# Optimization experiments

Hardware: AMD Instinct MI355X
Metric: run time of the kernel (lower is better)

The kernel has to match this reference:

```python
import jax, jax.numpy as jnp
import numpy as np

EMBED_DIM = 1024
NUM_TOKENS = 32
TOKEN_DIM = 32  # ceil(1024/32)
CODEBOOK_SIZE = 256
BATCH = 32768
BETA = 0.25


def setup_inputs() -> dict:
    key = jax.random.key(0)
    ks = jax.random.split(key, 6)
    lim_e = 1.0 / np.sqrt(EMBED_DIM)
    lim_d = 1.0 / np.sqrt(NUM_TOKENS * TOKEN_DIM)
    lim_c = 1.0 / CODEBOOK_SIZE
    return {
        "skills": jax.random.normal(ks[0], (BATCH, EMBED_DIM), jnp.float32),
        "enc_w": jax.random.uniform(ks[1], (NUM_TOKENS * TOKEN_DIM, EMBED_DIM), jnp.float32, -lim_e, lim_e),
        "enc_b": jax.random.uniform(ks[2], (NUM_TOKENS * TOKEN_DIM,), jnp.float32, -lim_e, lim_e),
        "codebook": jax.random.uniform(ks[3], (CODEBOOK_SIZE, TOKEN_DIM), jnp.float32, -lim_c, lim_c),
        "dec_w": jax.random.uniform(ks[4], (EMBED_DIM, NUM_TOKENS * TOKEN_DIM), jnp.float32, -lim_d, lim_d),
        "dec_b": jax.random.uniform(ks[5], (EMBED_DIM,), jnp.float32, -lim_d, lim_d),
    }


def reference(skills, enc_w, enc_b, codebook, dec_w, dec_b):
    B = skills.shape[0]
    # encoder linear -> [B, num_tokens, token_dim]
    projected = (skills @ enc_w.T + enc_b).reshape(B, NUM_TOKENS, TOKEN_DIM)
    flat = projected.reshape(-1, TOKEN_DIM)  # [B*T, d]
    # squared-euclidean distances to codebook entries: [B*T, K]
    dists = (
        jnp.sum(flat * flat, axis=1, keepdims=True)
        - 2.0 * flat @ codebook.T
        + jnp.sum(codebook * codebook, axis=1)[None, :]
    )
    codes = jnp.argmin(dists, axis=1)  # [B*T]
    quantized = codebook[codes].reshape(B, NUM_TOKENS, TOKEN_DIM)
    # straight-through estimator
    st = projected + jax.lax.stop_gradient(quantized - projected)
    commitment = jnp.mean((projected - jax.lax.stop_gradient(quantized)) ** 2)
    codebook_loss = jnp.mean((quantized - jax.lax.stop_gradient(projected)) ** 2)
    vq_loss = codebook_loss + BETA * commitment
    reconstructed = st.reshape(B, NUM_TOKENS * TOKEN_DIM) @ dec_w.T + dec_b
    recon_loss = jnp.mean((reconstructed - skills) ** 2)
    loss = vq_loss + recon_loss
    return reconstructed, codes.reshape(B, NUM_TOKENS), loss
```

## Files before the change

kernel.cpp:

```cpp
#include <hip/hip_runtime.h>
#include <hip/hip_bf16.h>
#include <float.h>

#define NROWS 32768
#define EMB 1024
#define CBN 256
#define TD 32

#define OUT_CODES_OFF (33554432UL)
#define OUT_LOSS_OFF  (34603008UL)
#define TAU 1e-5f
#define INV_N (1.0f/33554432.0f)

typedef __attribute__((ext_vector_type(8))) short s16x8;
typedef __attribute__((ext_vector_type(4))) float f32x4;

__device__ __forceinline__ unsigned short bf16r(float x) {
    unsigned int u = __float_as_uint(x);
    unsigned int r = (u + 0x7FFFu + ((u >> 16) & 1u)) >> 16;
    return (unsigned short)r;
}
__device__ __forceinline__ float bf16f(unsigned short h) {
    return __uint_as_float(((unsigned int)h) << 16);
}
__device__ __forceinline__ void split8r(float4 v0, float4 v1, s16x8& h, s16x8& l) {
    float xs[8] = {v0.x, v0.y, v0.z, v0.w, v1.x, v1.y, v1.z, v1.w};
    #pragma unroll
    for (int e = 0; e < 8; ++e) {
        unsigned int u = __float_as_uint(xs[e]);
        unsigned short hh = (unsigned short)(u >> 16);
        h[e] = (short)hh;
        l[e] = (short)bf16r(xs[e] - bf16f(hh));
    }
}

__global__ void k_prep(const float* __restrict__ in,
                       unsigned short* __restrict__ hi,
                       unsigned short* __restrict__ lo,
                       int n8)
{
    const int i = blockIdx.x * 256 + threadIdx.x;
    if (i >= n8) return;
    const float4* p = (const float4*)(in + (size_t)i * 8);
    s16x8 h, l;
    split8r(p[0], p[1], h, l);
    *(s16x8*)(hi + (size_t)i * 8) = h;
    *(s16x8*)(lo + (size_t)i * 8) = l;
}

template <bool PREW>
__launch_bounds__(512, 1)
__global__ void k_enc(const unsigned short* __restrict__ s_hi,
                      const unsigned short* __restrict__ s_lo,
                      const float* __restrict__ enc_w,
                      const unsigned short* __restrict__ w_hi,
                      const unsigned short* __restrict__ w_lo,
                      const float* __restrict__ enc_b,
                      const float* __restrict__ cb_g,
                      float* __restrict__ out)
{
    __shared__ __align__(16) char smem[125952];
    typedef unsigned short (*pu40)[40];
    pu40 Ah = (pu40)(smem);
    pu40 Al = (pu40)(smem + 10240);
    pu40 Bh = (pu40)(smem + 20480);
    pu40 Bl = (pu40)(smem + 30720);
    pu40 Sh = (pu40)(smem);
    pu40 Sl = (pu40)(smem + 40960);
    pu40 Ch = (pu40)(smem + 81920);
    pu40 Cl = (pu40)(smem + 102400);
    float* cnb = (float*)(smem + 122880);
    float* Fv  = (float*)(smem + 123904);

    const int tid = threadIdx.x;
    const int r0 = blockIdx.x * 128;
    const int wid = tid >> 6, lane = tid & 63;
    const int wm = wid >> 1, wn = wid & 1;
    const int mbase = wm * 32, nbase = wn * 64;
    const int lhi = lane >> 4, llo = lane & 15;
    const int srow = tid >> 2, sq = tid & 3;

    if (tid < 256) {
        const float4* cr = (const float4*)&cb_g[tid * 32];
        float s = 0.f;
        #pragma unroll
        for (int i = 0; i < 8; ++i) {
            float4 v = cr[i];
            float c[4] = {v.x, v.y, v.z, v.w};
            #pragma unroll
            for (int e = 0; e < 4; ++e) {
                unsigned int u = __float_as_uint(c[e]);
                unsigned short hh = (unsigned short)(u >> 16);
                Ch[tid][i*4+e] = hh;
                Cl[tid][i*4+e] = bf16r(c[e] - bf16f(hh));
                s = fmaf(c[e], c[e], s);
            }
        }
        cnb[tid] = s;
    }
    __syncthreads();

    float vq_local = 0.f;
    f32x4 acc[2][4];
    s16x8 rah, ral, rbh, rbl;

    {
        const size_t aoff = (size_t)(r0 + srow) * 1024 + sq * 8;
        rah = *(const s16x8*)(s_hi + aoff);
        ral = *(const s16x8*)(s_lo + aoff);
        if (PREW) {
            const size_t boff = (size_t)srow * 1024 + sq * 8;
            rbh = *(const s16x8*)(w_hi + boff);
            rbl = *(const s16x8*)(w_lo + boff);
        } else {
            const float* bp = &enc_w[(size_t)srow * 1024 + sq * 8];
            split8r(*(const float4*)bp, *(const float4*)(bp + 4), rbh, rbl);
        }
    }

    for (int it = 0; it < 256; ++it) {
        const int nt = it >> 5, kt = it & 31;
        const int n0 = nt * 128;
        if (kt == 0) {
            #pragma unroll
            for (int mf = 0; mf < 2; ++mf)
                #pragma unroll
                for (int nf = 0; nf < 4; ++nf) acc[mf][nf] = (f32x4)0.f;
        }
        __syncthreads();
        *(s16x8*)&Ah[srow][sq * 8] = rah;
        *(s16x8*)&Al[srow][sq * 8] = ral;
        *(s16x8*)&Bh[srow][sq * 8] = rbh;
        *(s16x8*)&Bl[srow][sq * 8] = rbl;
        __syncthreads();
        if (it < 255) {
            const int it2 = it + 1, nt2 = it2 >> 5, kt2 = it2 & 31;
            const size_t aoff = (size_t)(r0 + srow) * 1024 + kt2 * 32 + sq * 8;
            rah = *(const s16x8*)(s_hi + aoff);
            ral = *(const s16x8*)(s_lo + aoff);
            if (PREW) {
                const size_t boff = (size_t)(nt2 * 128 + srow) * 1024 + kt2 * 32 + sq * 8;
                rbh = *(const s16x8*)(w_hi + boff);
                rbl = *(const s16x8*)(w_lo + boff);
            } else {
                const float* bp = &enc_w[(size_t)(nt2 * 128 + srow) * 1024 + kt2 * 32 + sq * 8];
                split8r(*(const float4*)bp, *(const float4*)(bp + 4), rbh, rbl);
            }
        }
        {
            s16x8 ah[2], al[2], bh[4], bl[4];
            #pragma unroll
            for (int mf = 0; mf < 2; ++mf) {
                const int row = mbase + mf * 16 + llo;
                ah[mf] = *(s16x8*)&Ah[row][lhi * 8];
                al[mf] = *(s16x8*)&Al[row][lhi * 8];
            }
            #pragma unroll
            for (int nf = 0; nf < 4; ++nf) {
                const int row = nbase + nf * 16 + llo;
                bh[nf] = *(s16x8*)&Bh[row][lhi * 8];
                bl[nf] = *(s16x8*)&Bl[row][lhi * 8];
            }
            #pragma unroll
            for (int mf = 0; mf < 2; ++mf)
                #pragma unroll
                for (int nf = 0; nf < 4; ++nf) {
                    acc[mf][nf] = __builtin_amdgcn_mfma_f32_16x16x32_bf16(ah[mf], bh[nf], acc[mf][nf], 0, 0, 0);
                    acc[mf][nf] = __builtin_amdgcn_mfma_f32_16x16x32_bf16(ah[mf], bl[nf], acc[mf][nf], 0, 0, 0);
                    acc[mf][nf] = __builtin_amdgcn_mfma_f32_16x16x32_bf16(al[mf], bh[nf], acc[mf][nf], 0, 0, 0);
                }
        }

        if (kt == 31) {
            __syncthreads();
            float fp[2][4][2];
            #pragma unroll
            for (int mf = 0; mf < 2; ++mf)
                #pragma unroll
                for (int r = 0; r < 4; ++r) { fp[mf][r][0] = 0.f; fp[mf][r][1] = 0.f; }

            #pragma unroll
            for (int mf = 0; mf < 2; ++mf)
                #pragma unroll
                for (int nf = 0; nf < 4; ++nf) {
                    const int n_local = nbase + nf * 16 + llo;
                    const float bias = enc_b[n0 + n_local];
                    const int tl = wn * 2 + (nf >> 1);
                    const int d = ((nf & 1) << 4) + llo;
                    #pragma unroll
                    for (int r = 0; r < 4; ++r) {
                        const int m_local = mbase + mf * 16 + lhi * 4 + r;
                        float val = acc[mf][nf][r] + bias;
                        unsigned int u = __float_as_uint(val);
                        unsigned short hh = (unsigned short)(u >> 16);
                        Sh[m_local * 4 + tl][d] = hh;
                        Sl[m_local * 4 + tl][d] = bf16r(val - bf16f(hh));
                        fp[mf][r][nf >> 1] = fmaf(val, val, fp[mf][r][nf >> 1]);
                    }
                }
            #pragma unroll
            for (int mf = 0; mf < 2; ++mf)
                #pragma unroll
                for (int r = 0; r < 4; ++r)
                    #pragma unroll
                    for (int tt = 0; tt < 2; ++tt) {
                        float f = fp[mf][r][tt];
                        f += __shfl_xor(f, 1); f += __shfl_xor(f, 2);
                        f += __shfl_xor(f, 4); f += __shfl_xor(f, 8);
                        if (llo == 0)
                            Fv[(mbase + mf * 16 + lhi * 4 + r) * 4 + wn * 2 + tt] = f;
                    }
            __syncthreads();

            #pragma unroll
            for (int gi = 0; gi < 4; ++gi) {
                const int g = wid * 4 + gi;
                const int tokrow = g * 16 + llo;
                s16x8 fh = *(s16x8*)&Sh[tokrow][lhi * 8];
                s16x8 fl = *(s16x8*)&Sl[tokrow][lhi * 8];
                float s1[4], s2[4]; int bj[4];
                #pragma unroll
                for (int r = 0; r < 4; ++r) { s1[r] = FLT_MAX; s2[r] = FLT_MAX; bj[r] = 0; }
                for (int jb = 0; jb < 16; ++jb) {
                    const int j = jb * 16 + llo;
                    s16x8 ch = *(s16x8*)&Ch[j][lhi * 8];
                    s16x8 cl = *(s16x8*)&Cl[j][lhi * 8];
                    f32x4 sc = (f32x4)0.f;
                    sc = __builtin_amdgcn_mfma_f32_16x16x32_bf16(fh, ch, sc, 0, 0, 0);
                    sc = __builtin_amdgcn_mfma_f32_16x16x32_bf16(fh, cl, sc, 0, 0, 0);
                    sc = __builtin_amdgcn_mfma_f32_16x16x32_bf16(fl, ch, sc, 0, 0, 0);
                    const float cnv = cnb[j];
                    #pragma unroll
                    for (int r = 0; r < 4; ++r) {
                        float s = fmaf(-2.f, sc[r], cnv);
                        if (s < s1[r])      { s2[r] = s1[r]; s1[r] = s; bj[r] = j; }
                        else if (s < s2[r]) { s2[r] = s; }
                    }
                }
                #pragma unroll
                for (int r = 0; r < 4; ++r) {
                    float a1 = s1[r], a2 = s2[r]; int aj = bj[r];
                    #pragma unroll
                    for (int off = 1; off <= 8; off <<= 1) {
                        float o1 = __shfl_xor(a1, off);
                        float o2 = __shfl_xor(a2, off);
                        int   oj = __shfl_xor(aj, off);
                        if (o1 < a1) { a2 = fminf(a1, o2); a1 = o1; aj = oj; }
                        else         { a2 = fminf(o1, a2); }
                    }
                    if (llo == 0) {
                        const int tok_local = g * 16 + lhi * 4 + r;
                        const float F = Fv[tok_local];
                        float cv = (a2 - a1 < TAU) ? (float)(aj + 512) : (float)aj;
                        const size_t tok = (size_t)(r0 + (tok_local >> 2)) * 32 + nt * 4 + (tok_local & 3);
                        out[OUT_CODES_OFF + tok] = cv;
                        vq_local += F + a1;
                    }
                }
            }
        }
    }
    {
        float v = vq_local;
        #pragma unroll
        for (int off = 32; off >= 1; off >>= 1) v += __shfl_xor(v, off);
        if (lane == 0) atomicAdd(&out[OUT_LOSS_OFF], v * (1.25f * INV_N));
    }
}

__launch_bounds__(256)
__global__ void k_fix(const float* __restrict__ skills,
                      const float* __restrict__ enc_w,
                      const float* __restrict__ enc_b,
                      const float* __restrict__ cb_g,
                      float* __restrict__ codes)
{
    __shared__ unsigned int cnt;
    __shared__ unsigned short list[256];

    const int tid = threadIdx.x;
    const int base = blockIdx.x * 256;

    if (tid == 0) cnt = 0;
    __syncthreads();
    {
        const int c = (int)codes[base + tid];
        if (c >= 512) {
            unsigned int ix = atomicAdd(&cnt, 1u);
            list[ix] = (unsigned short)tid;
        }
    }
    __syncthreads();
    const unsigned int n = cnt;
    if (n == 0) return;

    const int wv = tid >> 6, lane = tid & 63;
    const int d = lane & 31;

    for (unsigned int i = wv; i < n; i += 4) {
        const int tok = base + (int)list[i];
        const int row = tok >> 5;
        const int t   = tok & 31;

        const float4* s4 = (const float4*)&skills[(size_t)row * 1024];
        const float4* w4 = (const float4*)&enc_w[(size_t)(t * 32 + d) * 1024];
        float v1 = 0.f, v2 = 0.f, v3 = 0.f;
        for (int q = 0; q < 96; ++q) {
            float4 a = s4[q], b = w4[q];
            v1 = fmaf(a.x, b.x, v1); v1 = fmaf(a.y, b.y, v1);
            v1 = fmaf(a.z, b.z, v1); v1 = fmaf(a.w, b.w, v1);
        }
        for (int q = 96; q < 192; ++q) {
            float4 a = s4[q], b = w4[q];
            v2 = fmaf(a.x, b.x, v2); v2 = fmaf(a.y, b.y, v2);
            v2 = fmaf(a.z, b.z, v2); v2 = fmaf(a.w, b.w, v2);
        }
        for (int q = 192; q < 256; ++q) {
            float4 a = s4[q], b = w4[q];
            v3 = fmaf(a.x, b.x, v3); v3 = fmaf(a.y, b.y, v3);
            v3 = fmaf(a.z, b.z, v3); v3 = fmaf(a.w, b.w, v3);
        }
        const float pd = ((v1 + v2) + v3) + enc_b[t * 32 + d];

        float pv[32];
        #pragma unroll
        for (int dd = 0; dd < 32; ++dd) pv[dd] = __shfl(pd, dd);

        float F;
        {
            float s[32];
            #pragma unroll
            for (int dd = 0; dd < 32; ++dd) s[dd] = pv[dd] * pv[dd];
            float r[8];
            #pragma unroll
            for (int j = 0; j < 8; ++j) r[j] = ((s[j] + s[8+j]) + s[16+j]) + s[24+j];
            F = ((r[0] + r[1]) + (r[2] + r[3])) + ((r[4] + r[5]) + (r[6] + r[7]));
        }

        float bs = FLT_MAX; int bj = 0;
        for (int m = 0; m < 4; ++m) {
            const int j = m * 64 + lane;
            const float* cj = &cb_g[j * 32];
            float g = 0.f;
            #pragma unroll
            for (int dd = 0; dd < 32; ++dd) g = fmaf(pv[dd], cj[dd], g);
            float cs[32];
            #pragma unroll
            for (int dd = 0; dd < 32; ++dd) cs[dd] = cj[dd] * cj[dd];
            float r[8];
            #pragma unroll
            for (int jj = 0; jj < 8; ++jj) r[jj] = ((cs[jj] + cs[8+jj]) + cs[16+jj]) + cs[24+jj];
            float cn = ((r[0] + r[1]) + (r[2] + r[3])) + ((r[4] + r[5]) + (r[6] + r[7]));
            float dist = (F - 2.0f * g) + cn;
            if (dist < bs) { bs = dist; bj = j; }
        }
        #pragma unroll
        for (int off = 32; off >= 1; off >>= 1) {
            float os = __shfl_xor(bs, off);
            int   oj = __shfl_xor(bj, off);
            if (os < bs || (os == bs && oj < bj)) { bs = os; bj = oj; }
        }
        if (lane == 0) codes[tok] = (float)bj;
    }
}

__launch_bounds__(512)
__global__ void k_dec(const float* __restrict__ skills,
                      const float* __restrict__ cb_g,
                      const float* __restrict__ dec_w,
                      const float* __restrict__ dec_b,
                      const float* __restrict__ codes,
                      float* __restrict__ recon,
                      float* __restrict__ loss_out)
{
    __shared__ unsigned short Qt[128][40], Wt[128][40];

    const int tid = threadIdx.x;
    const int r0 = (blockIdx.x >> 3) * 128;
    const int n0 = (blockIdx.x & 7) * 128;
    const int wid = tid >> 6, lane = tid & 63;
    const int wm = wid >> 1, wn = wid & 1;
    const int mbase = wm * 32, nbase = wn * 64;
    const int lhi = lane >> 4, llo = lane & 15;
    const int srow = tid >> 2, sq = tid & 3;

    f32x4 acc[2][4];
    #pragma unroll
    for (int mf = 0; mf < 2; ++mf)
        #pragma unroll
        for (int nf = 0; nf < 4; ++nf) acc[mf][nf] = (f32x4)0.f;

    float4 q0, q1, w0, w1;
    int cnext;
    {
        const int c0 = ((int)codes[(size_t)(r0 + srow) * 32 + 0]) & 255;
        const float* cp = &cb_g[c0 * 32 + sq * 8];
        q0 = *(const float4*)cp; q1 = *(const float4*)(cp + 4);
        const float* wp = &dec_w[(size_t)(n0 + srow) * 1024 + sq * 8];
        w0 = *(const float4*)wp; w1 = *(const float4*)(wp + 4);
        cnext = ((int)codes[(size_t)(r0 + srow) * 32 + 1]) & 255;
    }

    for (int t = 0; t < 32; ++t) {
        __syncthreads();
        {
            float xs[8] = {q0.x, q0.y, q0.z, q0.w, q1.x, q1.y, q1.z, q1.w};
            s16x8 h;
            #pragma unroll
            for (int e = 0; e < 8; ++e) h[e] = (short)bf16r(xs[e]);
            *(s16x8*)&Qt[srow][sq * 8] = h;
            float ys[8] = {w0.x, w0.y, w0.z, w0.w, w1.x, w1.y, w1.z, w1.w};
            #pragma unroll
            for (int e = 0; e < 8; ++e) h[e] = (short)bf16r(ys[e]);
            *(s16x8*)&Wt[srow][sq * 8] = h;
        }
        __syncthreads();
        if (t < 31) {
            const float* cp = &cb_g[cnext * 32 + sq * 8];
            q0 = *(const float4*)cp; q1 = *(const float4*)(cp + 4);
            const float* wp = &dec_w[(size_t)(n0 + srow) * 1024 + (t + 1) * 32 + sq * 8];
            w0 = *(const float4*)wp; w1 = *(const float4*)(wp + 4);
            if (t < 30) cnext = ((int)codes[(size_t)(r0 + srow) * 32 + t + 2]) & 255;
        }
        s16x8 aq[2], bw[4];
        #pragma unroll
        for (int mf = 0; mf < 2; ++mf)
            aq[mf] = *(s16x8*)&Qt[mbase + mf * 16 + llo][lhi * 8];
        #pragma unroll
        for (int nf = 0; nf < 4; ++nf)
            bw[nf] = *(s16x8*)&Wt[nbase + nf * 16 + llo][lhi * 8];
        #pragma unroll
        for (int mf = 0; mf < 2; ++mf)
            #pragma unroll
            for (int nf = 0; nf < 4; ++nf)
                acc[mf][nf] = __builtin_amdgcn_mfma_f32_16x16x32_bf16(aq[mf], bw[nf], acc[mf][nf], 0, 0, 0);
    }

    float lsum = 0.f;
    #pragma unroll
    for (int mf = 0; mf < 2; ++mf)
        #pragma unroll
        for (int nf = 0; nf < 4; ++nf) {
            const int col = n0 + nbase + nf * 16 + llo;
            const float bias = dec_b[col];
            #pragma unroll
            for (int r = 0; r < 4; ++r) {
                const int row = r0 + mbase + mf * 16 + lhi * 4 + r;
                float rv = acc[mf][nf][r] + bias;
                float dv = rv - skills[(size_t)row * 1024 + col];
                lsum = fmaf(dv, dv, lsum);
                recon[(size_t)row * 1024 + col] = rv;
            }
        }
    #pragma unroll
    for (int off = 32; off >= 1; off >>= 1) lsum += __shfl_xor(lsum, off);
    if (lane == 0) atomicAdd(loss_out, lsum * INV_N);
}

extern "C" void kernel_launch(void* const* d_in, const int* in_sizes, int n_in,
                              void* d_out, int out_size, void* d_ws, size_t ws_size,
                              hipStream_t stream)
{
    const float* skills = (const float*)d_in[0];
    const float* enc_w  = (const float*)d_in[1];
    const float* enc_b  = (const float*)d_in[2];
    const float* cbg    = (const float*)d_in[3];
    const float* dec_w  = (const float*)d_in[4];
    const float* dec_b  = (const float*)d_in[5];
    float* out = (float*)d_out;

    unsigned short* s_hi = (unsigned short*)out;
    unsigned short* s_lo = s_hi + 33554432UL;

    hipMemsetAsync(out + OUT_LOSS_OFF, 0, 4, stream);
    k_prep<<<dim3(16384), dim3(256), 0, stream>>>(skills, s_hi, s_lo, 4194304);

    const bool prew = (ws_size >= (4UL * 1048576UL + 64UL));
    unsigned short* w_hi = (unsigned short*)d_ws;
    unsigned short* w_lo = w_hi + 1048576UL;
    if (prew) {
        k_prep<<<dim3(512), dim3(256), 0, stream>>>(enc_w, w_hi, w_lo, 131072);
        k_enc<true><<<dim3(256), dim3(512), 0, stream>>>(s_hi, s_lo, enc_w, w_hi, w_lo,
                                                         enc_b, cbg, out);
    } else {
        k_enc<false><<<dim3(256), dim3(512), 0, stream>>>(s_hi, s_lo, enc_w, w_hi, w_lo,
                                                          enc_b, cbg, out);
    }
    k_fix<<<dim3(4096), dim3(256), 0, stream>>>(skills, enc_w, enc_b, cbg, out + OUT_CODES_OFF);
    k_dec<<<dim3(2048), dim3(512), 0, stream>>>(skills, cbg, dec_w, dec_b,
                                                out + OUT_CODES_OFF, out, out + OUT_LOSS_OFF);
}
```

Baseline: 947.1 us.

## Fuse skills bf16 split into encoder, widen N tile to 256, swizzle LDS

Removes the separate k_prep pass over skills, which wrote hi/lo bf16 copies. The encoder now loads fp32 skills directly and splits them in registers before the LDS store. The encoder N tile doubles to 256 (8 MFMA fragments per wave), halving the number of passes over the A rows. LDS uses an XOR-swizzled layout without padding, shrinking shared memory so launch bounds can allow 2 blocks per CU. The codebook argmin runs in two halves per 256-wide tile, which adds syncs and register pressure.

```diff
diff --git a/kernel.cpp b/kernel.cpp
--- a/kernel.cpp
+++ b/kernel.cpp
@@ -1,11 +1,6 @@
 #include <hip/hip_runtime.h>
 #include <hip/hip_bf16.h>
 #include <float.h>
-
-#define NROWS 32768
-#define EMB 1024
-#define CBN 256
-#define TD 32
 
 #define OUT_CODES_OFF (33554432UL)
 #define OUT_LOSS_OFF  (34603008UL)
@@ -49,9 +44,8 @@
 }
 
 template <bool PREW>
-__launch_bounds__(512, 1)
-__global__ void k_enc(const unsigned short* __restrict__ s_hi,
-                      const unsigned short* __restrict__ s_lo,
+__launch_bounds__(512, 2)
+__global__ void k_enc(const float* __restrict__ skills,
                       const float* __restrict__ enc_w,
                       const unsigned short* __restrict__ w_hi,
                       const unsigned short* __restrict__ w_lo,
@@ -59,26 +53,18 @@
                       const float* __restrict__ cb_g,
                       float* __restrict__ out)
 {
-    __shared__ __align__(16) char smem[125952];
-    typedef unsigned short (*pu40)[40];
-    pu40 Ah = (pu40)(smem);
-    pu40 Al = (pu40)(smem + 10240);
-    pu40 Bh = (pu40)(smem + 20480);
-    pu40 Bl = (pu40)(smem + 30720);
-    pu40 Sh = (pu40)(smem);
-    pu40 Sl = (pu40)(smem + 40960);
-    pu40 Ch = (pu40)(smem + 81920);
-    pu40 Cl = (pu40)(smem + 102400);
-    float* cnb = (float*)(smem + 122880);
-    float* Fv  = (float*)(smem + 123904);
+    __shared__ __align__(16) unsigned short us[50688];
+    float* cnb = (float*)(us + 49152);
+    float* Fv  = (float*)(us + 49664);
 
     const int tid = threadIdx.x;
     const int r0 = blockIdx.x * 128;
     const int wid = tid >> 6, lane = tid & 63;
     const int wm = wid >> 1, wn = wid & 1;
-    const int mbase = wm * 32, nbase = wn * 64;
+    const int mbase = wm * 32;
     const int lhi = lane >> 4, llo = lane & 15;
-    const int srow = tid >> 2, sq = tid & 3;
+    const int rowA = tid >> 2, kcA = tid & 3;
+    const int rowB = tid & 255, selB = tid >> 8;
 
     if (tid < 256) {
         const float4* cr = (const float4*)&cb_g[tid * 32];
@@ -89,10 +75,12 @@
             float c[4] = {v.x, v.y, v.z, v.w};
             #pragma unroll
             for (int e = 0; e < 4; ++e) {
+                const int d = i * 4 + e, kc = d >> 3, e8 = d & 7;
+                const int phys = tid ^ (kc << 2);
                 unsigned int u = __float_as_uint(c[e]);
                 unsigned short hh = (unsigned short)(u >> 16);
-                Ch[tid][i*4+e] = hh;
-                Cl[tid][i*4+e] = bf16r(c[e] - bf16f(hh));
+                us[8 * (4096 + kc * 256 + phys) + e8] = hh;
+                us[8 * (5120 + kc * 256 + phys) + e8] = bf16r(c[e] - bf16f(hh));
                 s = fmaf(c[e], c[e], s);
             }
         }
@@ -101,162 +89,196 @@
     __syncthreads();
 
     float vq_local = 0.f;
-    f32x4 acc[2][4];
-    s16x8 rah, ral, rbh, rbl;
+    f32x4 acc[2][8];
+    float4 pa0, pa1;
+    s16x8 pb[4];
+    float4 pbf[4];
 
     {
-        const size_t aoff = (size_t)(r0 + srow) * 1024 + sq * 8;
-        rah = *(const s16x8*)(s_hi + aoff);
-        ral = *(const s16x8*)(s_lo + aoff);
+        const float* ap = &skills[(size_t)(r0 + rowA) * 1024 + kcA * 8];
+        pa0 = *(const float4*)ap; pa1 = *(const float4*)(ap + 4);
         if (PREW) {
-            const size_t boff = (size_t)srow * 1024 + sq * 8;
-            rbh = *(const s16x8*)(w_hi + boff);
-            rbl = *(const s16x8*)(w_lo + boff);
+            const unsigned short* wp = (selB ? w_lo : w_hi) + (size_t)rowB * 1024;
+            #pragma unroll
+            for (int kc = 0; kc < 4; ++kc) pb[kc] = *(const s16x8*)(wp + kc * 8);
         } else {
-            const float* bp = &enc_w[(size_t)srow * 1024 + sq * 8];
-            split8r(*(const float4*)bp, *(const float4*)(bp + 4), rbh, rbl);
-        }
-    }
-
-    for (int it = 0; it < 256; ++it) {
+            const float* bp = &enc_w[(size_t)rowB * 1024 + selB * 16];
+            #pragma unroll
+            for (int q = 0; q < 4; ++q) pbf[q] = ((const float4*)bp)[q];
+        }
+    }
+
+    for (int it = 0; it < 128; ++it) {
         const int nt = it >> 5, kt = it & 31;
-        const int n0 = nt * 128;
+        const int n0 = nt * 256;
         if (kt == 0) {
             #pragma unroll
             for (int mf = 0; mf < 2; ++mf)
                 #pragma unroll
-                for (int nf = 0; nf < 4; ++nf) acc[mf][nf] = (f32x4)0.f;
+                for (int nf = 0; nf < 8; ++nf) acc[mf][nf] = (f32x4)0.f;
         }
         __syncthreads();
-        *(s16x8*)&Ah[srow][sq * 8] = rah;
-        *(s16x8*)&Al[srow][sq * 8] = ral;
-        *(s16x8*)&Bh[srow][sq * 8] = rbh;
-        *(s16x8*)&Bl[srow][sq * 8] = rbl;
+        {
+            s16x8 h, l; split8r(pa0, pa1, h, l);
+            const int phys = rowA ^ (kcA << 2);
+            *(s16x8*)(us + 8 * (kcA * 128 + phys)) = h;
+            *(s16x8*)(us + 8 * (512 + kcA * 128 + phys)) = l;
+        }
+        if (PREW) {
+            const int base = selB ? 2048 : 1024;
+            #pragma unroll
+            for (int kc = 0; kc < 4; ++kc) {
+                const int phys = rowB ^ (kc << 2);
+                *(s16x8*)(us + 8 * (base + kc * 256 + phys)) = pb[kc];
+            }
+        } else {
+            #pragma unroll
+            for (int kk = 0; kk < 2; ++kk) {
+                const int kc = selB * 2 + kk;
+                s16x8 h, l; split8r(pbf[kk * 2], pbf[kk * 2 + 1], h, l);
+                const int phys = rowB ^ (kc << 2);
+                *(s16x8*)(us + 8 * (1024 + kc * 256 + phys)) = h;
+                *(s16x8*)(us + 8 * (2048 + kc * 256 + phys)) = l;
+            }
+        }
         __syncthreads();
-        if (it < 255) {
+        if (it < 127) {
             const int it2 = it + 1, nt2 = it2 >> 5, kt2 = it2 & 31;
-            const size_t aoff = (size_t)(r0 + srow) * 1024 + kt2 * 32 + sq * 8;
-            rah = *(const s16x8*)(s_hi + aoff);
-            ral = *(const s16x8*)(s_lo + aoff);
+            const float* ap = &skills[(size_t)(r0 + rowA) * 1024 + kt2 * 32 + kcA * 8];
+            pa0 = *(const float4*)ap; pa1 = *(const float4*)(ap + 4);
             if (PREW) {
-                const size_t boff = (size_t)(nt2 * 128 + srow) * 1024 + kt2 * 32 + sq * 8;
-                rbh = *(const s16x8*)(w_hi + boff);
-                rbl = *(const s16x8*)(w_lo + boff);
+                const unsigned short* wp = (selB ? w_lo : w_hi)
+                    + (size_t)(nt2 * 256 + rowB) * 1024 + kt2 * 32;
+                #pragma unroll
+                for (int kc = 0; kc < 4; ++kc) pb[kc] = *(const s16x8*)(wp + kc * 8);
             } else {
-                const float* bp = &enc_w[(size_t)(nt2 * 128 + srow) * 1024 + kt2 * 32 + sq * 8];
-                split8r(*(const float4*)bp, *(const float4*)(bp + 4), rbh, rbl);
+                const float* bp = &enc_w[(size_t)(nt2 * 256 + rowB) * 1024 + kt2 * 32 + selB * 16];
+                #pragma unroll
+                for (int q = 0; q < 4; ++q) pbf[q] = ((const float4*)bp)[q];
             }
         }
         {
-            s16x8 ah[2], al[2], bh[4], bl[4];
+            s16x8 ah[2], al[2];
             #pragma unroll
             for (int mf = 0; mf < 2; ++mf) {
-                const int row = mbase + mf * 16 + llo;
-                ah[mf] = *(s16x8*)&Ah[row][lhi * 8];
-                al[mf] = *(s16x8*)&Al[row][lhi * 8];
-            }
-            #pragma unroll
-            for (int nf = 0; nf < 4; ++nf) {
-                const int row = nbase + nf * 16 + llo;
-                bh[nf] = *(s16x8*)&Bh[row][lhi * 8];
-                bl[nf] = *(s16x8*)&Bl[row][lhi * 8];
-            }
-            #pragma unroll
-            for (int mf = 0; mf < 2; ++mf)
-                #pragma unroll
-                for (int nf = 0; nf < 4; ++nf) {
-                    acc[mf][nf] = __builtin_amdgcn_mfma_f32_16x16x32_bf16(ah[mf], bh[nf], acc[mf][nf], 0, 0, 0);
-                    acc[mf][nf] = __builtin_amdgcn_mfma_f32_16x16x32_bf16(ah[mf], bl[nf], acc[mf][nf], 0, 0, 0);
-                    acc[mf][nf] = __builtin_amdgcn_mfma_f32_16x16x32_bf16(al[mf], bh[nf], acc[mf][nf], 0, 0, 0);
+                const int phys = (mbase + mf * 16 + llo) ^ (lhi << 2);
+                ah[mf] = *(s16x8*)(us + 8 * (lhi * 128 + phys));
+                al[mf] = *(s16x8*)(us + 8 * (512 + lhi * 128 + phys));
+            }
+            #pragma unroll
+            for (int nf = 0; nf < 8; ++nf) {
+                const int phys = (wn * 128 + nf * 16 + llo) ^ (lhi << 2);
+                s16x8 bh = *(s16x8*)(us + 8 * (1024 + lhi * 256 + phys));
+                s16x8 bl = *(s16x8*)(us + 8 * (2048 + lhi * 256 + phys));
+                #pragma unroll
+                for (int mf = 0; mf < 2; ++mf) {
+                    acc[mf][nf] = __builtin_amdgcn_mfma_f32_16x16x32_bf16(ah[mf], bh, acc[mf][nf], 0, 0, 0);
+                    acc[mf][nf] = __builtin_amdgcn_mfma_f32_16x16x32_bf16(ah[mf], bl, acc[mf][nf], 0, 0, 0);
+                    acc[mf][nf] = __builtin_amdgcn_mfma_f32_16x16x32_bf16(al[mf], bh, acc[mf][nf], 0, 0, 0);
                 }
+            }
         }
 
         if (kt == 31) {
-            __syncthreads();
-            float fp[2][4][2];
-            #pragma unroll
-            for (int mf = 0; mf < 2; ++mf)
-                #pragma unroll
-                for (int r = 0; r < 4; ++r) { fp[mf][r][0] = 0.f; fp[mf][r][1] = 0.f; }
-
-            #pragma unroll
-            for (int mf = 0; mf < 2; ++mf)
-                #pragma unroll
-                for (int nf = 0; nf < 4; ++nf) {
-                    const int n_local = nbase + nf * 16 + llo;
-                    const float bias = enc_b[n0 + n_local];
-                    const int tl = wn * 2 + (nf >> 1);
-                    const int d = ((nf & 1) << 4) + llo;
+            for (int h = 0; h < 2; ++h) {
+                __syncthreads();
+                if (wn == h) {
+                    float fp[2][4][4];
+                    #pragma unroll
+                    for (int mf = 0; mf < 2; ++mf)
+                        #pragma unroll
+                        for (int r = 0; r < 4; ++r)
+                            #pragma unroll
+                            for (int tl = 0; tl < 4; ++tl) fp[mf][r][tl] = 0.f;
+                    #pragma unroll
+                    for (int mf = 0; mf < 2; ++mf)
+                        #pragma unroll
+                        for (int nf = 0; nf < 8; ++nf) {
+                            const int col = nf * 16 + llo;
+                            const int tl = col >> 5, d = col & 31, kc = d >> 3, e8 = d & 7;
+                            const float bias = enc_b[n0 + h * 128 + col];
+                            #pragma unroll
+                            for (int r = 0; r < 4; ++r) {
+                                const int m_local = mbase + mf * 16 + lhi * 4 + r;
+                                float val = acc[mf][nf][r] + bias;
+                                unsigned int u = __float_as_uint(val);
+                                unsigned short hh = (unsigned short)(u >> 16);
+                                const int tokr = m_local * 4 + tl;
+                                const int phys = tokr ^ (kc << 2);
+                                us[8 * (kc * 512 + phys) + e8] = hh;
+                                us[8 * (2048 + kc * 512 + phys) + e8] = bf16r(val - bf16f(hh));
+                                fp[mf][r][tl] = fmaf(val, val, fp[mf][r][tl]);
+                            }
+                        }
+                    #pragma unroll
+                    for (int mf = 0; mf < 2; ++mf)
+                        #pragma unroll
+                        for (int r = 0; r < 4; ++r)
+                            #pragma unroll
+                            for (int tl = 0; tl < 4; ++tl) {
+                                float f = fp[mf][r][tl];
+                                f += __shfl_xor(f, 1); f += __shfl_xor(f, 2);
+                                f += __shfl_xor(f, 4); f += __shfl_xor(f, 8);
+                                if (llo == 0)
+                                    Fv[(mbase + mf * 16 + lhi * 4 + r) * 4 + tl] = f;
+                            }
+                }
+                __syncthreads();
+                s16x8 fh[4], fl[4];
+                #pragma unroll
+                for (int gi = 0; gi < 4; ++gi) {
+                    const int tokr = (wid * 4 + gi) * 16 + llo;
+                    const int phys = tokr ^ (lhi << 2);
+                    fh[gi] = *(s16x8*)(us + 8 * (lhi * 512 + phys));
+                    fl[gi] = *(s16x8*)(us + 8 * (2048 + lhi * 512 + phys));
+                }
+                float s1[4][4], s2[4][4]; int bj[4][4];
+                #pragma unroll
+                for (int gi = 0; gi < 4; ++gi)
+                    #pragma unroll
+                    for (int r = 0; r < 4; ++r) { s1[gi][r] = FLT_MAX; s2[gi][r] = FLT_MAX; bj[gi][r] = 0; }
+                for (int jb = 0; jb < 16; ++jb) {
+                    const int physj = (jb * 16 + llo) ^ (lhi << 2);
+                    s16x8 ch = *(s16x8*)(us + 8 * (4096 + lhi * 256 + physj));
+                    s16x8 cl = *(s16x8*)(us + 8 * (5120 + lhi * 256 + physj));
+                    const float cnv = cnb[jb * 16 + llo];
+                    #pragma unroll
+                    for (int gi = 0; gi < 4; ++gi) {
+                        f32x4 sc = (f32x4)0.f;
+                        sc = __builtin_amdgcn_mfma_f32_16x16x32_bf16(fh[gi], ch, sc, 0, 0, 0);
+                        sc = __builtin_amdgcn_mfma_f32_16x16x32_bf16(fh[gi], cl, sc, 0, 0, 0);
+                        sc = __builtin_amdgcn_mfma_f32_16x16x32_bf16(fl[gi], ch, sc, 0, 0, 0);
+                        #pragma unroll
+                        for (int r = 0; r < 4; ++r) {
+                            float s = fmaf(-2.f, sc[r], cnv);
+                            if (s < s1[gi][r])      { s2[gi][r] = s1[gi][r]; s1[gi][r] = s; bj[gi][r] = jb * 16 + llo; }
+                            else if (s < s2[gi][r]) { s2[gi][r] = s; }
+                        }
+                    }
+                }
+                #pragma unroll
+                for (int gi = 0; gi < 4; ++gi)
                     #pragma unroll
                     for (int r = 0; r < 4; ++r) {
-                        const int m_local = mbase + mf * 16 + lhi * 4 + r;
-                        float val = acc[mf][nf][r] + bias;
-                        unsigned int u = __float_as_uint(val);
-                        unsigned short hh = (unsigned short)(u >> 16);
-                        Sh[m_local * 4 + tl][d] = hh;
-                        Sl[m_local * 4 + tl][d] = bf16r(val - bf16f(hh));
-                        fp[mf][r][nf >> 1] = fmaf(val, val, fp[mf][r][nf >> 1]);
+                        float a1 = s1[gi][r], a2 = s2[gi][r]; int aj = bj[gi][r];
+                        #pragma unroll
+                        for (int off = 1; off <= 8; off <<= 1) {
+                            float o1 = __shfl_xor(a1, off);
+                            float o2 = __shfl_xor(a2, off);
+                            int   oj = __shfl_xor(aj, off);
+                            if (o1 < a1) { a2 = fminf(a1, o2); a1 = o1; aj = oj; }
+                            else         { a2 = fminf(o1, a2); }
+                        }
+                        if (llo == 0) {
+                            const int tok_local = (wid * 4 + gi) * 16 + lhi * 4 + r;
+                            const float F = Fv[tok_local];
+                            float cv = (a2 - a1 < TAU) ? (float)(aj + 512) : (float)aj;
+                            const size_t tok = (size_t)(r0 + (tok_local >> 2)) * 32
+                                               + nt * 8 + h * 4 + (tok_local & 3);
+                            out[OUT_CODES_OFF + tok] = cv;
+                            vq_local += F + a1;
+                        }
                     }
-                }
-            #pragma unroll
-            for (int mf = 0; mf < 2; ++mf)
-                #pragma unroll
-                for (int r = 0; r < 4; ++r)
-                    #pragma unroll
-                    for (int tt = 0; tt < 2; ++tt) {
-                        float f = fp[mf][r][tt];
-                        f += __shfl_xor(f, 1); f += __shfl_xor(f, 2);
-                        f += __shfl_xor(f, 4); f += __shfl_xor(f, 8);
-                        if (llo == 0)
-                            Fv[(mbase + mf * 16 + lhi * 4 + r) * 4 + wn * 2 + tt] = f;
-                    }
-            __syncthreads();
-
-            #pragma unroll
-            for (int gi = 0; gi < 4; ++gi) {
-                const int g = wid * 4 + gi;
-                const int tokrow = g * 16 + llo;
-                s16x8 fh = *(s16x8*)&Sh[tokrow][lhi * 8];
-                s16x8 fl = *(s16x8*)&Sl[tokrow][lhi * 8];
-                float s1[4], s2[4]; int bj[4];
-                #pragma unroll
-                for (int r = 0; r < 4; ++r) { s1[r] = FLT_MAX; s2[r] = FLT_MAX; bj[r] = 0; }
-                for (int jb = 0; jb < 16; ++jb) {
-                    const int j = jb * 16 + llo;
-                    s16x8 ch = *(s16x8*)&Ch[j][lhi * 8];
-                    s16x8 cl = *(s16x8*)&Cl[j][lhi * 8];
-                    f32x4 sc = (f32x4)0.f;
-                    sc = __builtin_amdgcn_mfma_f32_16x16x32_bf16(fh, ch, sc, 0, 0, 0);
-                    sc = __builtin_amdgcn_mfma_f32_16x16x32_bf16(fh, cl, sc, 0, 0, 0);
-                    sc = __builtin_amdgcn_mfma_f32_16x16x32_bf16(fl, ch, sc, 0, 0, 0);
-                    const float cnv = cnb[j];
-                    #pragma unroll
-                    for (int r = 0; r < 4; ++r) {
-                        float s = fmaf(-2.f, sc[r], cnv);
-                        if (s < s1[r])      { s2[r] = s1[r]; s1[r] = s; bj[r] = j; }
-                        else if (s < s2[r]) { s2[r] = s; }
-                    }
-                }
-                #pragma unroll
-                for (int r = 0; r < 4; ++r) {
-                    float a1 = s1[r], a2 = s2[r]; int aj = bj[r];
-                    #pragma unroll
-                    for (int off = 1; off <= 8; off <<= 1) {
-                        float o1 = __shfl_xor(a1, off);
-                        float o2 = __shfl_xor(a2, off);
-                        int   oj = __shfl_xor(aj, off);
-                        if (o1 < a1) { a2 = fminf(a1, o2); a1 = o1; aj = oj; }
-                        else         { a2 = fminf(o1, a2); }
-                    }
-                    if (llo == 0) {
-                        const int tok_local = g * 16 + lhi * 4 + r;
-                        const float F = Fv[tok_local];
-                        float cv = (a2 - a1 < TAU) ? (float)(aj + 512) : (float)aj;
-                        const size_t tok = (size_t)(r0 + (tok_local >> 2)) * 32 + nt * 4 + (tok_local & 3);
-                        out[OUT_CODES_OFF + tok] = cv;
-                        vq_local += F + a1;
-                    }
-                }
             }
         }
     }
@@ -469,21 +491,17 @@
     const float* dec_b  = (const float*)d_in[5];
     float* out = (float*)d_out;
 
-    unsigned short* s_hi = (unsigned short*)out;
-    unsigned short* s_lo = s_hi + 33554432UL;
-
     hipMemsetAsync(out + OUT_LOSS_OFF, 0, 4, stream);
-    k_prep<<<dim3(16384), dim3(256), 0, stream>>>(skills, s_hi, s_lo, 4194304);
 
     const bool prew = (ws_size >= (4UL * 1048576UL + 64UL));
     unsigned short* w_hi = (unsigned short*)d_ws;
     unsigned short* w_lo = w_hi + 1048576UL;
     if (prew) {
         k_prep<<<dim3(512), dim3(256), 0, stream>>>(enc_w, w_hi, w_lo, 131072);
-        k_enc<true><<<dim3(256), dim3(512), 0, stream>>>(s_hi, s_lo, enc_w, w_hi, w_lo,
+        k_enc<true><<<dim3(256), dim3(512), 0, stream>>>(skills, enc_w, w_hi, w_lo,
                                                          enc_b, cbg, out);
     } else {
-        k_enc<false><<<dim3(256), dim3(512), 0, stream>>>(s_hi, s_lo, enc_w, w_hi, w_lo,
+        k_enc<false><<<dim3(256), dim3(512), 0, stream>>>(skills, enc_w, w_hi, w_lo,
                                                           enc_b, cbg, out);
     }
     k_fix<<<dim3(4096), dim3(256), 0, stream>>>(skills, enc_w, enc_b, cbg, out + OUT_CODES_OFF);
```

Result: slower. 2.242 ms (+136.7%).
